# Optimization experiments

Measured on AMD Instinct MI355X. Metric: run time of the kernel, lower is better.

The kernel has to match this reference:

```python
import jax, jax.numpy as jnp
import numpy as np

FEATURES, HIDDEN, ITERS = 64, 128, 3
BS, N = 64, 512
TEMP = 0.01  # NegativeSquare temperature


def position_encoding_init(n_position, d):
    pos = np.arange(n_position)[:, None].astype(np.float64)
    j = np.arange(d)[None, :]
    enc = pos / np.power(10000.0, 2 * (j // 2) / d)
    enc[0] = 0.0
    enc[1:, 0::2] = np.sin(enc[1:, 0::2])
    enc[1:, 1::2] = np.cos(enc[1:, 1::2])
    return jnp.asarray(enc, jnp.float32)


def setup_inputs() -> dict:
    key = jax.random.key(0)
    ks = jax.random.split(key, 32)
    g = lambda k, shp: 0.02 * jax.random.normal(k, shp, dtype=jnp.float32)
    inp = {
        'x': jax.random.normal(ks[0], (BS, N, FEATURES), dtype=jnp.float32),
        'mask': jnp.ones((BS, N, N), dtype=jnp.float32),
        # content embedding (1-layer MLP features->hidden, relu)
        'W_emb': g(ks[1], (FEATURES, HIDDEN)), 'b_emb': jnp.zeros((HIDDEN,), jnp.float32),
        # sinusoid positional table (trainable Parameter in torch)
        'pos_table': position_encoding_init(1000, HIDDEN),
        # per-iteration MP layers (untied): message MLP + GRU vertex update
        'Wm': g(ks[2], (ITERS, HIDDEN, HIDDEN)), 'bm': jnp.zeros((ITERS, HIDDEN), jnp.float32),
        'Wz': g(ks[3], (ITERS, HIDDEN, HIDDEN)), 'Uz': g(ks[4], (ITERS, HIDDEN, HIDDEN)), 'bz': jnp.zeros((ITERS, HIDDEN), jnp.float32),
        'Wr': g(ks[5], (ITERS, HIDDEN, HIDDEN)), 'Ur': g(ks[6], (ITERS, HIDDEN, HIDDEN)), 'br': jnp.zeros((ITERS, HIDDEN), jnp.float32),
        'Wh': g(ks[7], (ITERS, HIDDEN, HIDDEN)), 'Uh': g(ks[8], (ITERS, HIDDEN, HIDDEN)), 'bh': jnp.zeros((ITERS, HIDDEN), jnp.float32),
        # positional GRUUpdate(hidden, 3): input h (hidden) -> state s (3)
        'Wpz': g(ks[9], (HIDDEN, 3)), 'Upz': g(ks[10], (3, 3)), 'bpz': jnp.zeros((3,), jnp.float32),
        'Wpr': g(ks[11], (HIDDEN, 3)), 'Upr': g(ks[12], (3, 3)), 'bpr': jnp.zeros((3,), jnp.float32),
        'Wph': g(ks[13], (HIDDEN, 3)), 'Uph': g(ks[14], (3, 3)), 'bph': jnp.zeros((3,), jnp.float32),
    }
    return inp


def _adj(s, mask):
    # NegativeSquare: exp(-||s_i - s_j||^2 / temperature) * mask
    sq = jnp.sum(s * s, axis=-1)  # [b, n]
    d2 = sq[:, :, None] + sq[:, None, :] - 2.0 * jnp.einsum('bid,bjd->bij', s, s)
    return jnp.exp(-d2 / TEMP) * mask


def _spatial_variable(bs, n):
    idx = (jnp.arange(n, dtype=jnp.float32) - (n - 1) / 2.0) / n
    s = jnp.stack([idx, jnp.zeros(n, jnp.float32), jnp.zeros(n, jnp.float32)], axis=-1)
    return jnp.broadcast_to(s[None], (bs, n, 3))


def reference(x, mask, W_emb, b_emb, pos_table, Wm, bm, Wz, Uz, bz, Wr, Ur, br,
              Wh, Uh, bh, Wpz, Upz, bpz, Wpr, Upr, bpr, Wph, Uph, bph):
    bs, n, _ = x.shape
    iters = Wm.shape[0]
    h = jax.nn.relu(jnp.einsum('bnf,fh->bnh', x, W_emb) + b_emb)
    h = h + pos_table[:n][None]  # pos = arange(n)
    s = _spatial_variable(bs, n)
    A = _adj(s, mask)
    for i in range(iters):
        # message passing layer i
        m = jax.nn.relu(jnp.einsum('bnh,hk->bnk', h, Wm[i]) + bm[i])
        agg = jnp.einsum('bij,bjh->bih', A, m)
        z = jax.nn.sigmoid(agg @ Wz[i] + h @ Uz[i] + bz[i])
        r = jax.nn.sigmoid(agg @ Wr[i] + h @ Ur[i] + br[i])
        hh = jnp.tanh(agg @ Wh[i] + (r * h) @ Uh[i] + bh[i])
        h = (1.0 - z) * h + z * hh
        # positional GRU update: input h, state s
        zs = jax.nn.sigmoid(h @ Wpz + s @ Upz + bpz)
        rs = jax.nn.sigmoid(h @ Wpr + s @ Upr + bpr)
        ss = jnp.tanh(h @ Wph + (rs * s) @ Uph + bph)
        s = (1.0 - zs) * s + zs * ss
        A = _adj(s, mask)
    return A
```

## Files before the change

### kernel.cpp

```cpp
#include <hip/hip_runtime.h>
#include <math.h>

#define BSZ  64
#define NSEQ 512
#define FEAT 64
#define HID  128
#define NITER 3
#define RTOT (BSZ*NSEQ)
#define LDAP 136

typedef __attribute__((ext_vector_type(8))) short bf16x8;
typedef __attribute__((ext_vector_type(4))) float f32x4;
typedef unsigned int u32;


__device__ __forceinline__ float sigm(float v) {
  v = fminf(fmaxf(v, -30.f), 30.f);
  return 1.0f / (1.0f + __expf(-v));
}
__device__ __forceinline__ float tanh_fast(float v) {
  v = fminf(fmaxf(v, -15.f), 15.f);
  float e = __expf(2.0f * v);
  return (e - 1.0f) / (e + 1.0f);
}

__device__ __forceinline__ u32 pack_split(float a) {
  u32 ub = __float_as_uint(a);
  u32 hi = ub >> 16;
  float res = a - __uint_as_float(hi << 16);
  u32 lo = __float_as_uint(res) >> 16;
  return (hi << 16) | lo;
}
__device__ __forceinline__ float bf2f(short v) {
  return __uint_as_float(((u32)(unsigned short)v) << 16);
}

__device__ __forceinline__ f32x4 mfma3(bf16x8 ah, bf16x8 al, bf16x8 bh, bf16x8 bl, f32x4 c) {
  c = __builtin_amdgcn_mfma_f32_16x16x32_bf16(ah, bh, c, 0, 0, 0);
  c = __builtin_amdgcn_mfma_f32_16x16x32_bf16(ah, bl, c, 0, 0, 0);
  c = __builtin_amdgcn_mfma_f32_16x16x32_bf16(al, bh, c, 0, 0, 0);
  return c;
}

__device__ __forceinline__ void stage_planes(const u32* __restrict__ g, short* hiP, short* loP, int t) {
  const int row = t >> 3, col = (t & 7) * 16;
  const u32* src = g + (size_t)row * HID + col;
  #pragma unroll
  for (int i = 0; i < 4; ++i) {
    uint4 u = *(const uint4*)(src + i * 4);
    *(short4*)&hiP[row * LDAP + col + i * 4] =
        make_short4((short)(u.x >> 16), (short)(u.y >> 16), (short)(u.z >> 16), (short)(u.w >> 16));
    *(short4*)&loP[row * LDAP + col + i * 4] =
        make_short4((short)(u.x & 0xffff), (short)(u.y & 0xffff), (short)(u.z & 0xffff), (short)(u.w & 0xffff));
  }
}

#define GATE(ACC, AP, WB) do { \
  _Pragma("unroll") \
  for (int ks_ = 0; ks_ < 4; ++ks_) { \
    bf16x8 ah_ = *(bf16x8*)&P[AP][lrow][ks_*32 + kgrp]; \
    bf16x8 al_ = *(bf16x8*)&P[(AP)+1][lrow][ks_*32 + kgrp]; \
    _Pragma("unroll") \
    for (int nt_ = 0; nt_ < 4; ++nt_) { \
      const short* fb_ = (WB) + (((ks_*2 + nh)*4 + nt_) * 1024) + l * 8; \
      bf16x8 bh_ = *(const bf16x8*)fb_; \
      bf16x8 bl_ = *(const bf16x8*)(fb_ + 512); \
      ACC[nt_] = mfma3(ah_, al_, bh_, bl_, ACC[nt_]); \
    } \
  } \
} while (0)

__device__ __forceinline__ void micro4(const float4 a, const float4 b0, const float4 b1,
                                       const float4 b2, const float4 b3, float acc[4]) {
  acc[0] = fmaf(a.x, b0.x, acc[0]); acc[0] = fmaf(a.y, b1.x, acc[0]);
  acc[0] = fmaf(a.z, b2.x, acc[0]); acc[0] = fmaf(a.w, b3.x, acc[0]);
  acc[1] = fmaf(a.x, b0.y, acc[1]); acc[1] = fmaf(a.y, b1.y, acc[1]);
  acc[1] = fmaf(a.z, b2.y, acc[1]); acc[1] = fmaf(a.w, b3.y, acc[1]);
  acc[2] = fmaf(a.x, b0.z, acc[2]); acc[2] = fmaf(a.y, b1.z, acc[2]);
  acc[2] = fmaf(a.z, b2.z, acc[2]); acc[2] = fmaf(a.w, b3.z, acc[2]);
  acc[3] = fmaf(a.x, b0.w, acc[3]); acc[3] = fmaf(a.y, b1.w, acc[3]);
  acc[3] = fmaf(a.z, b2.w, acc[3]); acc[3] = fmaf(a.w, b3.w, acc[3]);
}


__global__ __launch_bounds__(256) void k_prep(
    const float* __restrict__ Wm, const float* __restrict__ Wz, const float* __restrict__ Uz,
    const float* __restrict__ Wr, const float* __restrict__ Ur, const float* __restrict__ Wh,
    const float* __restrict__ Uh, short* __restrict__ wpl) {
  __shared__ float Wl[HID * HID];
  const int t = threadIdx.x;
  const int m = blockIdx.x;
  const int g = m / 3, it = m - g * 3;
  const float* src;
  switch (g) { case 0: src = Wm; break; case 1: src = Wz; break; case 2: src = Uz; break;
               case 3: src = Wr; break; case 4: src = Ur; break; case 5: src = Wh; break;
               default: src = Uh; }
  src += (size_t)it * HID * HID;
  for (int i = t; i < HID * HID / 4; i += 256) ((float4*)Wl)[i] = ((const float4*)src)[i];
  __syncthreads();
  short* dst = wpl + (size_t)m * 32768;
  for (int s = t; s < 2048; s += 256) {
    const int lane = s & 63;
    const int blk = s >> 6;
    const int nt = blk & 3;
    const int nh = (blk >> 2) & 1;
    const int ks = blk >> 3;
    const int n = nh * 64 + nt * 16 + (lane & 15);
    const int k0 = ks * 32 + (lane >> 4) * 8;
    short h8[8], l8[8];
    #pragma unroll
    for (int j = 0; j < 8; ++j) {
      u32 pk = pack_split(Wl[(size_t)(k0 + j) * HID + n]);
      h8[j] = (short)(pk >> 16);
      l8[j] = (short)(pk & 0xffff);
    }
    short* o = dst + blk * 1024 + lane * 8;
    *(bf16x8*)o = *(bf16x8*)h8;
    *(bf16x8*)(o + 512) = *(bf16x8*)l8;
  }
}

__global__ __launch_bounds__(256) void k_embed(const float* __restrict__ x, const float* __restrict__ W,
                                               const float* __restrict__ bias, const float* __restrict__ pos,
                                               u32* __restrict__ hP) {
  __shared__ float xs[32][FEAT];
  const int t = threadIdx.x;
  const int row0 = blockIdx.x * 32;
  {
    const float4* xv = (const float4*)(x + (size_t)row0 * FEAT);
    float4* xd = (float4*)&xs[0][0];
    for (int i = t; i < 32 * FEAT / 4; i += 256) xd[i] = xv[i];
  }
  __syncthreads();
  const int c0 = (t & 31) * 4;
  const int r0 = (t >> 5) * 4;
  float acc[4][4] = {};
  #pragma unroll 2
  for (int k = 0; k < FEAT; k += 4) {
    float4 b0 = *(const float4*)&W[(k + 0) * HID + c0];
    float4 b1 = *(const float4*)&W[(k + 1) * HID + c0];
    float4 b2 = *(const float4*)&W[(k + 2) * HID + c0];
    float4 b3 = *(const float4*)&W[(k + 3) * HID + c0];
    float4 a0 = *(const float4*)&xs[r0 + 0][k];
    float4 a1 = *(const float4*)&xs[r0 + 1][k];
    float4 a2 = *(const float4*)&xs[r0 + 2][k];
    float4 a3 = *(const float4*)&xs[r0 + 3][k];
    micro4(a0, b0, b1, b2, b3, acc[0]);
    micro4(a1, b0, b1, b2, b3, acc[1]);
    micro4(a2, b0, b1, b2, b3, acc[2]);
    micro4(a3, b0, b1, b2, b3, acc[3]);
  }
  const float4 bv = *(const float4*)&bias[c0];
  #pragma unroll
  for (int r = 0; r < 4; ++r) {
    const int row = row0 + r0 + r;
    const int n = row & (NSEQ - 1);
    const float4 pv = *(const float4*)&pos[(size_t)n * HID + c0];
    uint4 pk;
    pk.x = pack_split(fmaxf(acc[r][0] + bv.x, 0.f) + pv.x);
    pk.y = pack_split(fmaxf(acc[r][1] + bv.y, 0.f) + pv.y);
    pk.z = pack_split(fmaxf(acc[r][2] + bv.z, 0.f) + pv.z);
    pk.w = pack_split(fmaxf(acc[r][3] + bv.w, 0.f) + pv.w);
    *(uint4*)&hP[(size_t)row * HID + c0] = pk;
  }
}

__global__ __launch_bounds__(256) void k_sinit(float* __restrict__ s) {
  const int i = blockIdx.x * 256 + threadIdx.x;
  if (i < RTOT) {
    const int n = i & (NSEQ - 1);
    s[(size_t)i * 3 + 0] = ((float)n - (NSEQ - 1) * 0.5f) / (float)NSEQ;
    s[(size_t)i * 3 + 1] = 0.f;
    s[(size_t)i * 3 + 2] = 0.f;
  }
}

__global__ __launch_bounds__(512) void k_msg(const u32* __restrict__ hP, const short* __restrict__ wpl,
                                             int iter, const float* __restrict__ bm,
                                             short* __restrict__ mtB) {
  __shared__ short P[2][64][LDAP];
  __shared__ short T[2][128][72];
  const int t = threadIdx.x;
  const int row0 = blockIdx.x * 64;
  stage_planes(hP + (size_t)row0 * HID, &P[0][0][0], &P[1][0][0], t);
  __syncthreads();
  const int l = t & 63, w = t >> 6;
  const int mt = w & 3, nh = w >> 2;
  const int lrow = mt * 16 + (l & 15);
  const int kgrp = (l >> 4) * 8;
  const int ncol = l & 15;
  f32x4 z4 = {0.f, 0.f, 0.f, 0.f};
  f32x4 acc[4];
  #pragma unroll
  for (int i = 0; i < 4; ++i) acc[i] = z4;
  GATE(acc, 0, wpl + (size_t)(0 * 3 + iter) * 32768);
  const int rbase = mt * 16 + (l >> 4) * 4;
  #pragma unroll
  for (int nt = 0; nt < 4; ++nt) {
    const int cc = nh * 64 + nt * 16 + ncol;
    const float bmc = bm[cc];
    #pragma unroll
    for (int q = 0; q < 4; ++q) {
      u32 pk = pack_split(fmaxf(acc[nt][q] + bmc, 0.f));
      T[0][cc][rbase + q] = (short)(pk >> 16);
      T[1][cc][rbase + q] = (short)(pk & 0xffff);
    }
  }
  __syncthreads();
  const int b = row0 >> 9, j0 = row0 & (NSEQ - 1);
  const int n = t >> 2, jq = (t & 3) * 16;
  const int nh2 = n >> 6, nt2 = (n >> 4) & 3;
  #pragma unroll
  for (int gch = 0; gch < 2; ++gch) {
    const int jj = jq + gch * 8;
    const int jt = (j0 + jj) >> 5;
    const int jjj = (j0 + jj) & 31;
    const int lane = (jjj >> 3) * 16 + (n & 15);
    #pragma unroll
    for (int pl = 0; pl < 2; ++pl) {
      size_t off = ((((((size_t)b * 16 + jt) * 2 + nh2) * 4 + nt2) * 2 + pl) * 64 + lane) * 8;
      *(bf16x8*)&mtB[off] = *(bf16x8*)&T[pl][n][jj];
    }
  }
}

__global__ __launch_bounds__(256) void k_agg(const float* __restrict__ s, const float* __restrict__ mask,
                                             const short* __restrict__ mtB, u32* __restrict__ aggP) {
  __shared__ float sj[NSEQ][3];
  const int t = threadIdx.x;
  const int b = blockIdx.x;
  const int i0 = blockIdx.y * 32;
  {
    const float* sp = s + (size_t)b * NSEQ * 3;
    for (int i = t; i < NSEQ * 3; i += 256) (&sj[0][0])[i] = sp[i];
  }
  __syncthreads();
  const int l = t & 63, w = t >> 6;
  const int mt = w & 1, nh = w >> 1;
  const int kgrp = (l >> 4) * 8, ncol = l & 15;
  const int arow = mt * 16 + (l & 15);
  const float six = sj[i0 + arow][0], siy = sj[i0 + arow][1], siz = sj[i0 + arow][2];
  const float* mrow = mask + ((size_t)b * NSEQ + i0 + arow) * NSEQ;
  f32x4 z4 = {0.f, 0.f, 0.f, 0.f};
  f32x4 acc[4];
  #pragma unroll
  for (int i = 0; i < 4; ++i) acc[i] = z4;
  const short* mtb = mtB + (size_t)b * 131072;
  #pragma unroll 2
  for (int jt = 0; jt < 16; ++jt) {
    const int j0 = jt * 32 + kgrp;
    const float4 mk0 = *(const float4*)&mrow[j0];
    const float4 mk1 = *(const float4*)&mrow[j0 + 4];
    const float mv[8] = {mk0.x, mk0.y, mk0.z, mk0.w, mk1.x, mk1.y, mk1.z, mk1.w};
    short ha[8], la[8];
    #pragma unroll
    for (int j = 0; j < 8; ++j) {
      const int jj = j0 + j;
      const float dx = six - sj[jj][0], dy = siy - sj[jj][1], dz = siz - sj[jj][2];
      const u32 pk = pack_split(__expf(-100.0f * (dx * dx + dy * dy + dz * dz)) * mv[j]);
      ha[j] = (short)(pk >> 16);
      la[j] = (short)(pk & 0xffff);
    }
    const bf16x8 ah = *(bf16x8*)ha;
    const bf16x8 al = *(bf16x8*)la;
    #pragma unroll
    for (int nt = 0; nt < 4; ++nt) {
      const short* fb = mtb + ((((size_t)jt * 2 + nh) * 4 + nt) * 2) * 512 + l * 8;
      acc[nt] = mfma3(ah, al, *(const bf16x8*)fb, *(const bf16x8*)(fb + 512), acc[nt]);
    }
  }
  #pragma unroll
  for (int nt = 0; nt < 4; ++nt) {
    const int cc = nh * 64 + nt * 16 + ncol;
    #pragma unroll
    for (int q = 0; q < 4; ++q) {
      const int grow = i0 + mt * 16 + (l >> 4) * 4 + q;
      aggP[((size_t)b * NSEQ + grow) * HID + cc] = pack_split(acc[nt][q]);
    }
  }
}

__global__ __launch_bounds__(512) void k_zrc(
    const u32* __restrict__ aggP, u32* __restrict__ hP,
    const short* __restrict__ wpl, int iter,
    const float* __restrict__ bz, const float* __restrict__ br, const float* __restrict__ bhh) {
  __shared__ short P[4][64][LDAP];
  const int t = threadIdx.x;
  const int row0 = blockIdx.x * 64;
  stage_planes(aggP + (size_t)row0 * HID, &P[0][0][0], &P[1][0][0], t);
  stage_planes(hP + (size_t)row0 * HID, &P[2][0][0], &P[3][0][0], t);
  __syncthreads();
  const int l = t & 63, w = t >> 6;
  const int mt = w & 3, nh = w >> 2;
  const int lrow = mt * 16 + (l & 15);
  const int kgrp = (l >> 4) * 8;
  const int ncol = l & 15;
  f32x4 z4 = {0.f, 0.f, 0.f, 0.f};
  f32x4 accz[4], accr[4];
  #pragma unroll
  for (int i = 0; i < 4; ++i) { accz[i] = z4; accr[i] = z4; }
  #pragma unroll 1
  for (int g = 0; g < 4; ++g) {
    const short* WB = wpl + (size_t)((g + 1) * 3 + iter) * 32768;
    const int ap = (g & 1) * 2;
    if (g < 2) { GATE(accz, ap, WB); }
    else       { GATE(accr, ap, WB); }
  }
  const int rbase = mt * 16 + (l >> 4) * 4;
  float hreg[4][4];
  float rhv[4][4];
  #pragma unroll
  for (int nt = 0; nt < 4; ++nt) {
    const int cc = nh * 64 + nt * 16 + ncol;
    const float brc = br[cc];
    #pragma unroll
    for (int q = 0; q < 4; ++q) {
      float hv = bf2f(P[2][rbase + q][cc]) + bf2f(P[3][rbase + q][cc]);
      hreg[nt][q] = hv;
      rhv[nt][q] = sigm(accr[nt][q] + brc) * hv;
    }
  }
  __syncthreads();
  #pragma unroll
  for (int nt = 0; nt < 4; ++nt) {
    const int cc = nh * 64 + nt * 16 + ncol;
    #pragma unroll
    for (int q = 0; q < 4; ++q) {
      u32 pk = pack_split(rhv[nt][q]);
      P[2][rbase + q][cc] = (short)(pk >> 16);
      P[3][rbase + q][cc] = (short)(pk & 0xffff);
    }
  }
  __syncthreads();
  #pragma unroll
  for (int i = 0; i < 4; ++i) accr[i] = z4;
  GATE(accr, 0, wpl + (size_t)(5 * 3 + iter) * 32768);
  GATE(accr, 2, wpl + (size_t)(6 * 3 + iter) * 32768);
  #pragma unroll
  for (int nt = 0; nt < 4; ++nt) {
    const int cc = nh * 64 + nt * 16 + ncol;
    const float bzc = bz[cc], bhc = bhh[cc];
    #pragma unroll
    for (int q = 0; q < 4; ++q) {
      float z = sigm(accz[nt][q] + bzc);
      float cand = tanh_fast(accr[nt][q] + bhc);
      float hn = (1.f - z) * hreg[nt][q] + z * cand;
      hP[(size_t)(row0 + rbase + q) * HID + cc] = pack_split(hn);
    }
  }
}

__global__ __launch_bounds__(256) void k_posgru(const u32* __restrict__ hP, float* __restrict__ s,
    const float* __restrict__ Wpz, const float* __restrict__ Upz, const float* __restrict__ bpz,
    const float* __restrict__ Wpr, const float* __restrict__ Upr, const float* __restrict__ bpr,
    const float* __restrict__ Wph, const float* __restrict__ Uph, const float* __restrict__ bph) {
  const int lane = threadIdx.x & 63;
  const int w = threadIdx.x >> 6;
  const int row = blockIdx.x * 4 + w;
  const int k0 = lane * 2;
  const uint2 hv2 = *(const uint2*)&hP[(size_t)row * HID + k0];
  const float hx = bf2f((short)(hv2.x >> 16)) + bf2f((short)(hv2.x & 0xffff));
  const float hy = bf2f((short)(hv2.y >> 16)) + bf2f((short)(hv2.y & 0xffff));
  float p[9];
  #pragma unroll
  for (int c = 0; c < 3; ++c) {
    p[c]     = hx * Wpz[k0 * 3 + c] + hy * Wpz[(k0 + 1) * 3 + c];
    p[3 + c] = hx * Wpr[k0 * 3 + c] + hy * Wpr[(k0 + 1) * 3 + c];
    p[6 + c] = hx * Wph[k0 * 3 + c] + hy * Wph[(k0 + 1) * 3 + c];
  }
  #pragma unroll
  for (int off = 32; off > 0; off >>= 1) {
    #pragma unroll
    for (int q = 0; q < 9; ++q) p[q] += __shfl_xor(p[q], off, 64);
  }
  const float s0 = s[(size_t)row * 3 + 0], s1 = s[(size_t)row * 3 + 1], s2 = s[(size_t)row * 3 + 2];
  float zs[3], rs[3], ss[3];
  #pragma unroll
  for (int c = 0; c < 3; ++c) {
    zs[c] = sigm(p[c]     + s0 * Upz[c] + s1 * Upz[3 + c] + s2 * Upz[6 + c] + bpz[c]);
    rs[c] = sigm(p[3 + c] + s0 * Upr[c] + s1 * Upr[3 + c] + s2 * Upr[6 + c] + bpr[c]);
  }
  const float t0 = rs[0] * s0, t1 = rs[1] * s1, t2 = rs[2] * s2;
  #pragma unroll
  for (int c = 0; c < 3; ++c)
    ss[c] = tanh_fast(p[6 + c] + t0 * Uph[c] + t1 * Uph[3 + c] + t2 * Uph[6 + c] + bph[c]);
  if (lane == 0) {
    s[(size_t)row * 3 + 0] = (1.f - zs[0]) * s0 + zs[0] * ss[0];
    s[(size_t)row * 3 + 1] = (1.f - zs[1]) * s1 + zs[1] * ss[1];
    s[(size_t)row * 3 + 2] = (1.f - zs[2]) * s2 + zs[2] * ss[2];
  }
}

__global__ __launch_bounds__(256) void k_finalA(const float* __restrict__ s, const float* __restrict__ mask,
                                                float* __restrict__ A) {
  __shared__ float sj[NSEQ][3];
  const int t = threadIdx.x;
  const int b = blockIdx.x;
  const int i0 = blockIdx.y * 16;
  {
    const float* sp = s + (size_t)b * NSEQ * 3;
    for (int i = t; i < NSEQ * 3; i += 256) (&sj[0][0])[i] = sp[i];
  }
  __syncthreads();
  #pragma unroll
  for (int p = 0; p < 8; ++p) {
    const int e = t + p * 256;
    const int ii = e >> 7;
    const int j4 = (e & 127) * 4;
    const float six = sj[i0 + ii][0], siy = sj[i0 + ii][1], siz = sj[i0 + ii][2];
    const size_t base = ((size_t)b * NSEQ + i0 + ii) * NSEQ + j4;
    const float4 mk = *(const float4*)&mask[base];
    float4 o;
    { float dx = six - sj[j4+0][0], dy = siy - sj[j4+0][1], dz = siz - sj[j4+0][2];
      o.x = __expf(-100.0f*(dx*dx + dy*dy + dz*dz)) * mk.x; }
    { float dx = six - sj[j4+1][0], dy = siy - sj[j4+1][1], dz = siz - sj[j4+1][2];
      o.y = __expf(-100.0f*(dx*dx + dy*dy + dz*dz)) * mk.y; }
    { float dx = six - sj[j4+2][0], dy = siy - sj[j4+2][1], dz = siz - sj[j4+2][2];
      o.z = __expf(-100.0f*(dx*dx + dy*dy + dz*dz)) * mk.z; }
    { float dx = six - sj[j4+3][0], dy = siy - sj[j4+3][1], dz = siz - sj[j4+3][2];
      o.w = __expf(-100.0f*(dx*dx + dy*dy + dz*dz)) * mk.w; }
    *(float4*)&A[base] = o;
  }
}


extern "C" void kernel_launch(void* const* d_in, const int* in_sizes, int n_in,
                              void* d_out, int out_size, void* d_ws, size_t ws_size,
                              hipStream_t stream) {
  const float* x      = (const float*)d_in[0];
  const float* mask   = (const float*)d_in[1];
  const float* W_emb  = (const float*)d_in[2];
  const float* b_emb  = (const float*)d_in[3];
  const float* pos    = (const float*)d_in[4];
  const float* Wm     = (const float*)d_in[5];
  const float* bm     = (const float*)d_in[6];
  const float* Wz     = (const float*)d_in[7];
  const float* Uz     = (const float*)d_in[8];
  const float* bz     = (const float*)d_in[9];
  const float* Wr     = (const float*)d_in[10];
  const float* Ur     = (const float*)d_in[11];
  const float* br     = (const float*)d_in[12];
  const float* Wh     = (const float*)d_in[13];
  const float* Uh     = (const float*)d_in[14];
  const float* bh     = (const float*)d_in[15];
  const float* Wpz    = (const float*)d_in[16];
  const float* Upz    = (const float*)d_in[17];
  const float* bpz    = (const float*)d_in[18];
  const float* Wpr    = (const float*)d_in[19];
  const float* Upr    = (const float*)d_in[20];
  const float* bpr    = (const float*)d_in[21];
  const float* Wph    = (const float*)d_in[22];
  const float* Uph    = (const float*)d_in[23];
  const float* bph    = (const float*)d_in[24];

  u32*   hP = (u32*)d_ws;
  float* s  = (float*)d_ws + (size_t)RTOT * HID;
  float* ob   = (float*)d_out;
  u32*   aggP = (u32*)ob;
  short* mtB  = (short*)(ob + (size_t)RTOT * HID);
  short* wpl  = mtB + (size_t)BSZ * 131072;

  k_prep<<<21, 256, 0, stream>>>(Wm, Wz, Uz, Wr, Ur, Wh, Uh, wpl);
  k_embed<<<RTOT / 32, 256, 0, stream>>>(x, W_emb, b_emb, pos, hP);
  k_sinit<<<RTOT / 256, 256, 0, stream>>>(s);

  for (int i = 0; i < NITER; ++i) {
    const size_t bo = (size_t)i * HID;
    k_msg<<<RTOT / 64, 512, 0, stream>>>(hP, wpl, i, bm + bo, mtB);
    k_agg<<<dim3(BSZ, NSEQ / 32), 256, 0, stream>>>(s, mask, mtB, aggP);
    k_zrc<<<RTOT / 64, 512, 0, stream>>>(aggP, hP, wpl, i, bz + bo, br + bo, bh + bo);
    k_posgru<<<RTOT / 4, 256, 0, stream>>>(hP, s, Wpz, Upz, bpz, Wpr, Upr, bpr, Wph, Uph, bph);
  }
  k_finalA<<<dim3(BSZ, NSEQ / 16), 256, 0, stream>>>(s, mask, (float*)d_out);
}
```

Measured before the change: 525.0 us.

## Enlarge k_agg row tile to 64, compute each adjacency entry once, prefetch mask

Each k_agg block now covers 64 rows instead of 32, and each wave computes its 16 rows' adjacency values once for all 128 output columns (8 accumulators) rather than two waves recomputing the same exp values for separate column halves. Mask loads are software-prefetched one 128-column group ahead, and the positions are padded to float4 in shared memory so each is fetched with a single vector load. This removes duplicated exp and mask work and halves mtB re-reads per row, at the cost of more registers and half as many blocks in the grid.

```diff
diff --git a/kernel.cpp b/kernel.cpp
--- a/kernel.cpp
+++ b/kernel.cpp
@@ -226,56 +226,84 @@
 
 __global__ __launch_bounds__(256) void k_agg(const float* __restrict__ s, const float* __restrict__ mask,
                                              const short* __restrict__ mtB, u32* __restrict__ aggP) {
-  __shared__ float sj[NSEQ][3];
+  __shared__ float sj4[NSEQ][4];
   const int t = threadIdx.x;
   const int b = blockIdx.x;
-  const int i0 = blockIdx.y * 32;
+  const int i0 = blockIdx.y * 64;
   {
     const float* sp = s + (size_t)b * NSEQ * 3;
-    for (int i = t; i < NSEQ * 3; i += 256) (&sj[0][0])[i] = sp[i];
+    for (int i = t; i < NSEQ; i += 256) {
+      sj4[i][0] = sp[i * 3 + 0];
+      sj4[i][1] = sp[i * 3 + 1];
+      sj4[i][2] = sp[i * 3 + 2];
+      sj4[i][3] = 0.f;
+    }
   }
   __syncthreads();
   const int l = t & 63, w = t >> 6;
-  const int mt = w & 1, nh = w >> 1;
   const int kgrp = (l >> 4) * 8, ncol = l & 15;
-  const int arow = mt * 16 + (l & 15);
-  const float six = sj[i0 + arow][0], siy = sj[i0 + arow][1], siz = sj[i0 + arow][2];
+  const int arow = w * 16 + (l & 15);
+  const float six = sj4[i0 + arow][0], siy = sj4[i0 + arow][1], siz = sj4[i0 + arow][2];
   const float* mrow = mask + ((size_t)b * NSEQ + i0 + arow) * NSEQ;
   f32x4 z4 = {0.f, 0.f, 0.f, 0.f};
-  f32x4 acc[4];
-  #pragma unroll
-  for (int i = 0; i < 4; ++i) acc[i] = z4;
+  f32x4 acc[8];
+  #pragma unroll
+  for (int i = 0; i < 8; ++i) acc[i] = z4;
   const short* mtb = mtB + (size_t)b * 131072;
-  #pragma unroll 2
-  for (int jt = 0; jt < 16; ++jt) {
-    const int j0 = jt * 32 + kgrp;
-    const float4 mk0 = *(const float4*)&mrow[j0];
-    const float4 mk1 = *(const float4*)&mrow[j0 + 4];
-    const float mv[8] = {mk0.x, mk0.y, mk0.z, mk0.w, mk1.x, mk1.y, mk1.z, mk1.w};
-    short ha[8], la[8];
-    #pragma unroll
-    for (int j = 0; j < 8; ++j) {
-      const int jj = j0 + j;
-      const float dx = six - sj[jj][0], dy = siy - sj[jj][1], dz = siz - sj[jj][2];
-      const u32 pk = pack_split(__expf(-100.0f * (dx * dx + dy * dy + dz * dz)) * mv[j]);
-      ha[j] = (short)(pk >> 16);
-      la[j] = (short)(pk & 0xffff);
-    }
-    const bf16x8 ah = *(bf16x8*)ha;
-    const bf16x8 al = *(bf16x8*)la;
-    #pragma unroll
-    for (int nt = 0; nt < 4; ++nt) {
-      const short* fb = mtb + ((((size_t)jt * 2 + nh) * 4 + nt) * 2) * 512 + l * 8;
-      acc[nt] = mfma3(ah, al, *(const bf16x8*)fb, *(const bf16x8*)(fb + 512), acc[nt]);
-    }
-  }
-  #pragma unroll
-  for (int nt = 0; nt < 4; ++nt) {
-    const int cc = nh * 64 + nt * 16 + ncol;
+
+  float4 c[8];
+  #pragma unroll
+  for (int k = 0; k < 4; ++k) {
+    c[2 * k]     = *(const float4*)&mrow[k * 32 + kgrp];
+    c[2 * k + 1] = *(const float4*)&mrow[k * 32 + kgrp + 4];
+  }
+  #pragma unroll 1
+  for (int jg = 0; jg < 4; ++jg) {
+    float4 nx[8];
+    if (jg < 3) {
+      const int nb = (jg + 1) * 128;
+      #pragma unroll
+      for (int k = 0; k < 4; ++k) {
+        nx[2 * k]     = *(const float4*)&mrow[nb + k * 32 + kgrp];
+        nx[2 * k + 1] = *(const float4*)&mrow[nb + k * 32 + kgrp + 4];
+      }
+    }
+    #pragma unroll
+    for (int k = 0; k < 4; ++k) {
+      const int jt = jg * 4 + k;
+      const int j0 = jt * 32 + kgrp;
+      const float mv[8] = {c[2*k].x, c[2*k].y, c[2*k].z, c[2*k].w,
+                           c[2*k+1].x, c[2*k+1].y, c[2*k+1].z, c[2*k+1].w};
+      short ha[8], la[8];
+      #pragma unroll
+      for (int j = 0; j < 8; ++j) {
+        const float4 sv = *(const float4*)&sj4[j0 + j][0];
+        const float dx = six - sv.x, dy = siy - sv.y, dz = siz - sv.z;
+        const float d2 = dx * dx + dy * dy + dz * dz;
+        const u32 pk = pack_split(__expf(-100.0f * d2) * mv[j]);
+        ha[j] = (short)(pk >> 16);
+        la[j] = (short)(pk & 0xffff);
+      }
+      const bf16x8 ah = *(bf16x8*)ha;
+      const bf16x8 al = *(bf16x8*)la;
+      #pragma unroll
+      for (int n2 = 0; n2 < 8; ++n2) {
+        const short* fb = mtb + ((((size_t)jt * 2 + (n2 >> 2)) * 4 + (n2 & 3)) * 2) * 512 + l * 8;
+        acc[n2] = mfma3(ah, al, *(const bf16x8*)fb, *(const bf16x8*)(fb + 512), acc[n2]);
+      }
+    }
+    if (jg < 3) {
+      #pragma unroll
+      for (int q = 0; q < 8; ++q) c[q] = nx[q];
+    }
+  }
+  #pragma unroll
+  for (int n2 = 0; n2 < 8; ++n2) {
+    const int cc = (n2 >> 2) * 64 + (n2 & 3) * 16 + ncol;
     #pragma unroll
     for (int q = 0; q < 4; ++q) {
-      const int grow = i0 + mt * 16 + (l >> 4) * 4 + q;
-      aggP[((size_t)b * NSEQ + grow) * HID + cc] = pack_split(acc[nt][q]);
+      const int grow = i0 + w * 16 + (l >> 4) * 4 + q;
+      aggP[((size_t)b * NSEQ + grow) * HID + cc] = pack_split(acc[n2][q]);
     }
   }
 }
@@ -467,7 +495,7 @@
   for (int i = 0; i < NITER; ++i) {
     const size_t bo = (size_t)i * HID;
     k_msg<<<RTOT / 64, 512, 0, stream>>>(hP, wpl, i, bm + bo, mtB);
-    k_agg<<<dim3(BSZ, NSEQ / 32), 256, 0, stream>>>(s, mask, mtB, aggP);
+    k_agg<<<dim3(BSZ, NSEQ / 64), 256, 0, stream>>>(s, mask, mtB, aggP);
     k_zrc<<<RTOT / 64, 512, 0, stream>>>(aggP, hP, wpl, i, bz + bo, br + bo, bh + bo);
     k_posgru<<<RTOT / 4, 256, 0, stream>>>(hP, s, Wpz, Upz, bpz, Wpr, Upr, bpr, Wph, Uph, bph);
   }
```

After: 550.3 us. 1.05x slower.
